# Performance work log

Hardware: AMD Instinct MI355X
Metric: run time of the kernel (lower is better)

The kernel has to match this reference:

```python
import jax, jax.numpy as jnp
import numpy as np

B = 1048576
N_BINS = 128


def setup_inputs() -> dict:
    key = jax.random.key(0)
    k1, k2 = jax.random.split(key)
    # input: probabilities-ish in [0,1], shape [B, n_bins]
    inp = jax.random.uniform(k1, (B, N_BINS), dtype=jnp.float32)
    # bins: sorted bin edge values (sorted for realism; math doesn't require it)
    bins = jnp.sort(jax.random.normal(k2, (N_BINS,), dtype=jnp.float32))
    return {"input": inp, "bins": bins}


def reference(input, bins):
    # scores[:,0]=0; scores[:,i+1]=scores[:,i]+1-2*input[:,i]  == exclusive-prefixed cumsum
    deltas = 1.0 - 2.0 * input                      # [B, n]
    zeros = jnp.zeros((input.shape[0], 1), dtype=input.dtype)
    scores = jnp.concatenate([zeros, jnp.cumsum(deltas, axis=1)], axis=1)  # [B, n+1]
    indices = jnp.argmin(scores, axis=1)            # [B]
    bins_to_select = jnp.concatenate([bins[:1], bins, bins[-1:]])          # [n+2]
    chosen = (bins_to_select[indices] + bins_to_select[indices + 1]) * 0.5 # [B]
    return chosen[:, None]
```

## Files before the change

### kernel.cpp

```cpp
#include <hip/hip_runtime.h>


#define NBINS 128

__global__ __launch_bounds__(256) void fitstep_kernel(
    const float* __restrict__ inp,
    const float* __restrict__ bins,
    float* __restrict__ out,
    int nrows)
{
    int row = blockIdx.x * blockDim.x + threadIdx.x;
    if (row >= nrows) return;

    const float4* r4 = reinterpret_cast<const float4*>(inp + (size_t)row * NBINS);

    float score   = 0.0f;
    float best    = 0.0f;
    int   bestIdx = 0;

    #pragma unroll 8
    for (int j = 0; j < NBINS / 4; ++j) {
        float4 v = r4[j];
        float xs0 = v.x, xs1 = v.y, xs2 = v.z, xs3 = v.w;

        score += (1.0f - 2.0f * xs0);
        if (score < best) { best = score; bestIdx = j * 4 + 1; }
        score += (1.0f - 2.0f * xs1);
        if (score < best) { best = score; bestIdx = j * 4 + 2; }
        score += (1.0f - 2.0f * xs2);
        if (score < best) { best = score; bestIdx = j * 4 + 3; }
        score += (1.0f - 2.0f * xs3);
        if (score < best) { best = score; bestIdx = j * 4 + 4; }
    }

    int lo = bestIdx - 1; if (lo < 0) lo = 0;
    int hi = bestIdx;     if (hi > NBINS - 1) hi = NBINS - 1;
    out[row] = (bins[lo] + bins[hi]) * 0.5f;
}

extern "C" void kernel_launch(void* const* d_in, const int* in_sizes, int n_in,
                              void* d_out, int out_size, void* d_ws, size_t ws_size,
                              hipStream_t stream)
{
    const float* inp  = (const float*)d_in[0];
    const float* bins = (const float*)d_in[1];
    float* out = (float*)d_out;

    int nrows = in_sizes[0] / NBINS;
    int block = 256;
    int grid  = (nrows + block - 1) / block;

    fitstep_kernel<<<grid, block, 0, stream>>>(inp, bins, out, nrows);
}
```

Baseline: 100.7 us.

## Stage row chunks through double-buffered swizzled LDS for coalesced global loads

Each block now loads 256 rows cooperatively in 32-column chunks. Consecutive threads read contiguous 128-byte row segments, so global loads are coalesced, and the data is written to shared memory with an XOR swizzle to avoid bank conflicts. The next chunk is prefetched into registers while the current one is scanned from LDS, giving double buffering. This replaces the strided per-thread 512-byte row reads of the old kernel. In exchange it adds 64KB of LDS per block, which may limit occupancy, and a block-wide sync per chunk.

After: 94.65 us (median of 2 runs). 1.06x faster.

```diff
diff --git a/kernel.cpp b/kernel.cpp
--- a/kernel.cpp
+++ b/kernel.cpp
@@ -2,40 +2,102 @@
 
 
 #define NBINS 128
+#define ROWS  256
+#define CHUNK 32
+#define NCHUNK (NBINS / CHUNK)
 
-__global__ __launch_bounds__(256) void fitstep_kernel(
+__global__ __launch_bounds__(ROWS) void fitstep_kernel(
     const float* __restrict__ inp,
     const float* __restrict__ bins,
     float* __restrict__ out,
     int nrows)
 {
-    int row = blockIdx.x * blockDim.x + threadIdx.x;
-    if (row >= nrows) return;
+    __shared__ float lds[2][ROWS * CHUNK];
 
-    const float4* r4 = reinterpret_cast<const float4*>(inp + (size_t)row * NBINS);
+    const int t = threadIdx.x;
+    const size_t rowbase = (size_t)blockIdx.x * ROWS;
 
-    float score   = 0.0f;
-    float best    = 0.0f;
-    int   bestIdx = 0;
+    if (rowbase + ROWS <= (size_t)nrows) {
+        const float* base = inp + rowbase * NBINS;
+        float4 pf[8];
 
-    #pragma unroll 8
-    for (int j = 0; j < NBINS / 4; ++j) {
-        float4 v = r4[j];
-        float xs0 = v.x, xs1 = v.y, xs2 = v.z, xs3 = v.w;
+        #pragma unroll
+        for (int i = 0; i < 8; ++i) {
+            int f = i * ROWS + t;
+            int r = f >> 3, k = f & 7;
+            pf[i] = *reinterpret_cast<const float4*>(base + (size_t)r * NBINS + k * 4);
+        }
+        #pragma unroll
+        for (int i = 0; i < 8; ++i) {
+            int f = i * ROWS + t;
+            int r = f >> 3, k = f & 7;
+            int slot = k ^ (r & 7);
+            *reinterpret_cast<float4*>(&lds[0][r * CHUNK + slot * 4]) = pf[i];
+        }
+        __syncthreads();
 
-        score += (1.0f - 2.0f * xs0);
-        if (score < best) { best = score; bestIdx = j * 4 + 1; }
-        score += (1.0f - 2.0f * xs1);
-        if (score < best) { best = score; bestIdx = j * 4 + 2; }
-        score += (1.0f - 2.0f * xs2);
-        if (score < best) { best = score; bestIdx = j * 4 + 3; }
-        score += (1.0f - 2.0f * xs3);
-        if (score < best) { best = score; bestIdx = j * 4 + 4; }
+        float score = 0.0f, best = 0.0f;
+        int bestIdx = 0;
+
+        for (int c = 0; c < NCHUNK; ++c) {
+            const int buf = c & 1;
+
+            if (c + 1 < NCHUNK) {
+                #pragma unroll
+                for (int i = 0; i < 8; ++i) {
+                    int f = i * ROWS + t;
+                    int r = f >> 3, k = f & 7;
+                    pf[i] = *reinterpret_cast<const float4*>(
+                        base + (size_t)r * NBINS + (c + 1) * CHUNK + k * 4);
+                }
+            }
+
+            #pragma unroll
+            for (int j = 0; j < 8; ++j) {
+                int slot = j ^ (t & 7);
+                float4 v = *reinterpret_cast<const float4*>(
+                    &lds[buf][t * CHUNK + slot * 4]);
+                int colbase = c * CHUNK + j * 4;
+                score += (1.0f - 2.0f * v.x);
+                if (score < best) { best = score; bestIdx = colbase + 1; }
+                score += (1.0f - 2.0f * v.y);
+                if (score < best) { best = score; bestIdx = colbase + 2; }
+                score += (1.0f - 2.0f * v.z);
+                if (score < best) { best = score; bestIdx = colbase + 3; }
+                score += (1.0f - 2.0f * v.w);
+                if (score < best) { best = score; bestIdx = colbase + 4; }
+            }
+
+            if (c + 1 < NCHUNK) {
+                #pragma unroll
+                for (int i = 0; i < 8; ++i) {
+                    int f = i * ROWS + t;
+                    int r = f >> 3, k = f & 7;
+                    int slot = k ^ (r & 7);
+                    *reinterpret_cast<float4*>(
+                        &lds[buf ^ 1][r * CHUNK + slot * 4]) = pf[i];
+                }
+                __syncthreads();
+            }
+        }
+
+        int lo = bestIdx - 1; if (lo < 0) lo = 0;
+        int hi = bestIdx;     if (hi > NBINS - 1) hi = NBINS - 1;
+        out[rowbase + t] = (bins[lo] + bins[hi]) * 0.5f;
+    } else {
+        size_t row = rowbase + t;
+        if (row >= (size_t)nrows) return;
+        const float* rp = inp + row * NBINS;
+        float score = 0.0f, best = 0.0f;
+        int bestIdx = 0;
+        for (int j = 0; j < NBINS; ++j) {
+            score += (1.0f - 2.0f * rp[j]);
+            if (score < best) { best = score; bestIdx = j + 1; }
+        }
+        int lo = bestIdx - 1; if (lo < 0) lo = 0;
+        int hi = bestIdx;     if (hi > NBINS - 1) hi = NBINS - 1;
+        out[row] = (bins[lo] + bins[hi]) * 0.5f;
     }
-
-    int lo = bestIdx - 1; if (lo < 0) lo = 0;
-    int hi = bestIdx;     if (hi > NBINS - 1) hi = NBINS - 1;
-    out[row] = (bins[lo] + bins[hi]) * 0.5f;
 }
 
 extern "C" void kernel_launch(void* const* d_in, const int* in_sizes, int n_in,
@@ -47,8 +109,7 @@
     float* out = (float*)d_out;
 
     int nrows = in_sizes[0] / NBINS;
-    int block = 256;
-    int grid  = (nrows + block - 1) / block;
+    int grid  = (nrows + ROWS - 1) / ROWS;
 
-    fitstep_kernel<<<grid, block, 0, stream>>>(inp, bins, out, nrows);
+    fitstep_kernel<<<grid, ROWS, 0, stream>>>(inp, bins, out, nrows);
 }
```
